# Kernel tuning notes

Hardware: AMD Instinct MI355X
Metric: run time of the kernel (lower is better)

The kernel has to match this reference:

```python
import jax, jax.numpy as jnp
import numpy as np

CAPACITY_FACTOR = 1.0
MIN_CAPACITY = 4


def setup_inputs() -> dict:
    key = jax.random.key(0)
    ks = jax.random.split(key, 4)
    B, S, D, E, F = 4, 2048, 1024, 16, 4096
    hidden_states = jax.random.normal(ks[0], (B, S, D), dtype=jnp.float32)
    wg = jax.random.normal(ks[1], (D, E), dtype=jnp.float32) * 0.02
    w1 = jax.random.normal(ks[2], (E, D, F), dtype=jnp.float32) * (1.0 / np.sqrt(D))
    b1 = jnp.zeros((E, F), dtype=jnp.float32)
    w2 = jax.random.normal(ks[3], (E, F, D), dtype=jnp.float32) * (1.0 / np.sqrt(F))
    b2 = jnp.zeros((E, D), dtype=jnp.float32)
    return {"hidden_states": hidden_states, "wg": wg, "w1": w1, "b1": b1, "w2": w2, "b2": b2}


def reference(hidden_states, wg, w1, b1, w2, b2):
    B, S, D = hidden_states.shape
    x = hidden_states.reshape(-1, D)                      # [T, D] tokens
    T = x.shape[0]
    E = wg.shape[1]
    capacity = max(int(np.ceil(T / E * CAPACITY_FACTOR)), MIN_CAPACITY)  # static

    # ---- TopKGate (k=1, no noise, no RTS) ----
    logits = x @ wg                                       # [T, E]
    gates = jax.nn.softmax(logits, axis=-1)
    idx1 = jnp.argmax(gates, axis=1)                      # [T]
    mask1 = jax.nn.one_hot(idx1, E, dtype=gates.dtype)    # [T, E]
    exp_counts = jnp.sum(mask1, axis=0).astype(jnp.int32) # per-expert token counts

    # load-balancing aux loss
    me = jnp.mean(gates, axis=0)
    ce = jnp.mean(mask1, axis=0)
    l_aux = jnp.sum(me * ce) * E

    # slot assignment within each expert, drop overflow tokens
    locations1 = jnp.cumsum(mask1, axis=0) - 1.0          # [T, E]
    mask1 = mask1 * (locations1 < capacity).astype(gates.dtype)
    locations1_s = jnp.sum(locations1 * mask1, axis=1).astype(jnp.int32)  # [T]
    gates1 = gates * mask1                                # [T, E] gate prob of kept assignment

    loc_oh = jax.nn.one_hot(locations1_s, capacity, dtype=gates.dtype)    # [T, C]
    combine = jnp.einsum('te,tc->tec', gates1, loc_oh)    # [T, E, C]
    dispatch = (combine > 0).astype(x.dtype)              # [T, E, C]

    # ---- dispatch -> grouped expert FFN -> combine ----
    disp = jnp.einsum('tec,td->ecd', dispatch, x)         # [E, C, D]
    h = jax.nn.gelu(jnp.einsum('ecd,edf->ecf', disp, w1) + b1[:, None, :])
    eo = jnp.einsum('ecf,efd->ecd', h, w2) + b2[:, None, :]  # [E, C, D]
    out = jnp.einsum('tec,ecd->td', combine, eo).reshape(B, S, D)
    return out, l_aux, exp_counts
```

## Files before the change

### kernel.cpp

```cpp
#include <hip/hip_runtime.h>

typedef unsigned short u16;
typedef unsigned int   u32;
typedef unsigned long long u64;
typedef __attribute__((ext_vector_type(8))) __bf16 bf16x8;
typedef __attribute__((ext_vector_type(4))) float  f32x4;
typedef __attribute__((ext_vector_type(2))) u32    u32x2;

#define TOK 8192
#define DIM 1024
#define NE  16
#define NF  4096
#define CAP 512

#define BQ  288
#define BG  1184
#define BLSZ 9472

__device__ __forceinline__ u16 f2bf(float f) {
    u32 u = __float_as_uint(f);
    u32 r = (u + 0x7FFFu + ((u >> 16) & 1u)) >> 16;
    return (u16)r;
}

__device__ __forceinline__ float gelu_tanh(float x) {
    float u = 0.7978845608028654f * (x + 0.044715f * x * x * x);
    float t = __expf(-2.f * fabsf(u));
    float th = (1.f - t) / (1.f + t);
    th = (u < 0.f) ? -th : th;
    return 0.5f * x * (1.f + th);
}

__device__ __forceinline__ void gld16(const void* g, void* l) {
    __builtin_amdgcn_global_load_lds(
        (const __attribute__((address_space(1))) void*)g,
        (__attribute__((address_space(3))) void*)l, 16, 0, 0);
}

__device__ __forceinline__ u32 lds_addr(const void* p) {
    return (u32)(uintptr_t)(const __attribute__((address_space(3))) void*)p;
}

#define BFRAG2(BF0, BF1, A0, A1) do { \
    u32x2 l0_, h0_, l1_, h1_; \
    asm volatile("ds_read_b64_tr_b16 %0, %4\n\t" \
                 "ds_read_b64_tr_b16 %1, %4 offset:128\n\t" \
                 "ds_read_b64_tr_b16 %2, %5\n\t" \
                 "ds_read_b64_tr_b16 %3, %5 offset:128\n\t" \
                 "s_waitcnt lgkmcnt(0)" \
                 : "=&v"(l0_), "=&v"(h0_), "=&v"(l1_), "=&v"(h1_) \
                 : "v"(A0), "v"(A1) : "memory"); \
    union { u32 u[4]; bf16x8 v; } c0_, c1_; \
    c0_.u[0] = l0_[0]; c0_.u[1] = l0_[1]; c0_.u[2] = h0_[0]; c0_.u[3] = h0_[1]; \
    c1_.u[0] = l1_[0]; c1_.u[1] = l1_[1]; c1_.u[2] = h1_[0]; c1_.u[3] = h1_[1]; \
    (BF0) = c0_.v; (BF1) = c1_.v; } while (0)

__global__ void moe_wgT(const float* __restrict__ wg, float* __restrict__ wgT,
                        float* __restrict__ me_sums) {
    int i = blockIdx.x * 256 + threadIdx.x;
    if (i < NE) me_sums[i] = 0.f;
    int d = i >> 4, e = i & 15;
    wgT[(size_t)e * DIM + d] = wg[i];
}

__global__ void moe_gate(const float* __restrict__ x, const float* __restrict__ wgT,
                         int* __restrict__ eidx, float* __restrict__ gp,
                         float* __restrict__ me_sums) {
    __shared__ float lme[NE];
    const int tid = threadIdx.x;
    if (tid < NE) lme[tid] = 0.f;
    __syncthreads();
    const int tok = blockIdx.x * 16 + (tid >> 4);
    const int e   = tid & 15;
    const float4* xp = (const float4*)(x + (size_t)tok * DIM);
    const float4* wp = (const float4*)(wgT + (size_t)e * DIM);
    float acc = 0.f;
#pragma unroll 4
    for (int i = 0; i < DIM / 4; ++i) {
        float4 a = xp[i], b = wp[i];
        acc = fmaf(a.x, b.x, acc); acc = fmaf(a.y, b.y, acc);
        acc = fmaf(a.z, b.z, acc); acc = fmaf(a.w, b.w, acc);
    }
    float mx = acc;
    for (int off = 8; off; off >>= 1) mx = fmaxf(mx, __shfl_xor(mx, off, 16));
    float ex = __expf(acc - mx);
    float sum = ex;
    for (int off = 8; off; off >>= 1) sum += __shfl_xor(sum, off, 16);
    float p = ex / sum;
    atomicAdd(&lme[e], p);
    float bv = acc; int bi = e;
    for (int off = 8; off; off >>= 1) {
        float ov = __shfl_xor(bv, off, 16);
        int   oi = __shfl_xor(bi, off, 16);
        if (ov > bv || (ov == bv && oi < bi)) { bv = ov; bi = oi; }
    }
    float pw = __shfl(p, bi, 16);
    if (e == 0) { eidx[tok] = bi; gp[tok] = pw; }
    __syncthreads();
    if (tid < 16) atomicAdd(&me_sums[tid], lme[tid]);
}

__global__ void moe_scan(const int* __restrict__ eidx, const float* __restrict__ me_sums,
                         int* __restrict__ slot, int* __restrict__ tos,
                         float* __restrict__ tail ) {
    __shared__ int wcnt[16][16];
    __shared__ int base[16];
    const int tid = threadIdx.x, wid = tid >> 6, lane = tid & 63;
    if (tid < 16) base[tid] = 0;
    for (int i = tid; i < NE * CAP; i += 1024) tos[i] = -1;
    __syncthreads();
    const u64 below = ((u64)1 << lane) - 1;
    for (int chunk = 0; chunk < TOK / 1024; ++chunk) {
        int t = chunk * 1024 + tid;
        int e = eidx[t];
        int rank = 0;
#pragma unroll
        for (int ex = 0; ex < 16; ++ex) {
            u64 m = __ballot(e == ex);
            if (e == ex)    rank = __popcll(m & below);
            if (lane == ex) wcnt[wid][ex] = __popcll(m);
        }
        __syncthreads();
        int pre = base[e];
        for (int w = 0; w < wid; ++w) pre += wcnt[w][e];
        int s = pre + rank;
        slot[t] = s;
        if (s < CAP) tos[e * CAP + s] = t;
        __syncthreads();
        if (tid < 16) {
            int tot = 0;
            for (int w = 0; w < 16; ++w) tot += wcnt[w][tid];
            base[tid] += tot;
        }
        __syncthreads();
    }
    if (tid == 0) {
        float laux = 0.f;
        for (int e2 = 0; e2 < 16; ++e2) {
            float me = me_sums[e2] / (float)TOK;
            float ce = (float)base[e2] / (float)TOK;
            laux += me * ce;
        }
        tail[0] = laux * (float)NE;
    }
    if (tid < 16) tail[1 + tid] = (float)base[tid];
}

__global__ void moe_gather_zero(const float* __restrict__ x, const int* __restrict__ tos,
                                const int* __restrict__ slot, u16* __restrict__ Xg,
                                float* __restrict__ out) {
    const int b = blockIdx.x, tid = threadIdx.x;
    const int t = tos[b];
    float4 v = make_float4(0.f, 0.f, 0.f, 0.f);
    if (t >= 0) v = *(const float4*)(x + (size_t)t * DIM + tid * 4);
    u32 lo = (u32)f2bf(v.x) | ((u32)f2bf(v.y) << 16);
    u32 hi = (u32)f2bf(v.z) | ((u32)f2bf(v.w) << 16);
    *(uint2*)(Xg + (size_t)b * DIM + tid * 4) = make_uint2(lo, hi);
    if (slot[b] >= CAP)
        *(float4*)(out + (size_t)b * DIM + tid * 4) = make_float4(0.f, 0.f, 0.f, 0.f);
}

__global__ __launch_bounds__(512, 4) void moe_gemm1(const u16* __restrict__ Xg,
                                                    const float* __restrict__ w1,
                                                    const float* __restrict__ b1,
                                                    u16* __restrict__ H) {
    __shared__ alignas(16) u16 Als[2][8192];
    __shared__ alignas(16) u16 Bls[2][BLSZ / 2];
    const int tid = threadIdx.x, wave = tid >> 6, lane = tid & 63;
    const int flat = blockIdx.x;
    const int xcd  = flat & 7;
    const int slot = flat >> 3;
    const int e    = xcd * 2 + (slot >> 6);
    const int tile = slot & 63;
    const int bm   = tile & 1;
    const int bn   = tile >> 1;
    const int r4   = lane >> 2;
    const int gch  = (lane & 3) ^ ((lane >> 3) & 3);
    const u16* aSrc = Xg + (size_t)(e * 512 + bm * 256 + wave * 16 + r4) * DIM + gch * 8;
    const int bk = tid >> 4, bn8 = tid & 15;
    const float* bSrc = w1 + ((size_t)e * DIM + bk) * NF + bn * 128 + bn8 * 8;
    const int bwoff = (bn8 >> 1) * BG + (bk >> 3) * BQ + (bk & 7) * 32 + (bn8 & 1) * 16;
    const int wm = wave & 1, wn = wave >> 1;
    const int fr = lane & 15, fq = lane >> 4;
    const int rdoff = fr * 32 + (fq ^ ((fr >> 1) & 3)) * 8;
    const u32 ldsB = lds_addr(&Bls[0][0]);
    const int btr0 = (wn * 2 + 0) * BG + fq * BQ + fr * 2;
    const int btr1 = (wn * 2 + 1) * BG + fq * BQ + fr * 2;

    f32x4 acc[2][4][2] = {};
    float4 q0, q1;

#define STGA1(P, T) do { const int ko = (T) * 32; \
        u16* ad = &Als[P][wave * 512]; \
        gld16(aSrc + ko, ad); gld16(aSrc + 128 * DIM + ko, ad + 4096); } while (0)
#define BWR1(P) do { \
        u32 p0 = (u32)f2bf(q0.x) | ((u32)f2bf(q0.y) << 16); \
        u32 p1 = (u32)f2bf(q0.z) | ((u32)f2bf(q0.w) << 16); \
        u32 p2 = (u32)f2bf(q1.x) | ((u32)f2bf(q1.y) << 16); \
        u32 p3 = (u32)f2bf(q1.z) | ((u32)f2bf(q1.w) << 16); \
        *(uint4*)((char*)&Bls[0][0] + (P) * BLSZ + bwoff) = make_uint4(p0, p1, p2, p3); } while (0)

    const int NT = DIM / 32;
    STGA1(0, 0);
    q0 = *(const float4*)(bSrc); q1 = *(const float4*)(bSrc + 4);
    asm volatile("s_waitcnt vmcnt(0)" ::: "memory");
    BWR1(0);
    asm volatile("s_waitcnt lgkmcnt(0)" ::: "memory");
    __builtin_amdgcn_s_barrier();
    for (int t = 0; t < NT; ++t) {
        const int buf = t & 1;
        if (t + 1 < NT) {
            STGA1(buf ^ 1, t + 1);
            const float* s = bSrc + (size_t)(t + 1) * (32 * NF);
            q0 = *(const float4*)(s); q1 = *(const float4*)(s + 4);
        }
        bf16x8 aF[4], bF[2];
        const u32 bb = ldsB + buf * BLSZ;
        BFRAG2(bF[0], bF[1], bb + btr0, bb + btr1);
        const u16* Ab = &Als[buf][0];
#pragma unroll
        for (int i = 0; i < 4; ++i)
            aF[i] = *(const bf16x8*)(const void*)(Ab + (wm * 128 + i * 16) * 32 + rdoff);
        __builtin_amdgcn_sched_barrier(0);
        __builtin_amdgcn_s_setprio(1);
#pragma unroll
        for (int i = 0; i < 4; ++i)
#pragma unroll
            for (int j = 0; j < 2; ++j)
                acc[0][i][j] = __builtin_amdgcn_mfma_f32_16x16x32_bf16(aF[i], bF[j], acc[0][i][j], 0, 0, 0);
        __builtin_amdgcn_s_setprio(0);
#pragma unroll
        for (int i = 0; i < 4; ++i)
            aF[i] = *(const bf16x8*)(const void*)(Ab + (wm * 128 + 64 + i * 16) * 32 + rdoff);
        __builtin_amdgcn_s_setprio(1);
#pragma unroll
        for (int i = 0; i < 4; ++i)
#pragma unroll
            for (int j = 0; j < 2; ++j)
                acc[1][i][j] = __builtin_amdgcn_mfma_f32_16x16x32_bf16(aF[i], bF[j], acc[1][i][j], 0, 0, 0);
        __builtin_amdgcn_s_setprio(0);
        if (t + 1 < NT) {
            asm volatile("s_waitcnt vmcnt(0)" ::: "memory");
            BWR1(buf ^ 1);
        }
        asm volatile("s_waitcnt lgkmcnt(0)" ::: "memory");
        __builtin_amdgcn_s_barrier();
    }
#undef STGA1
#undef BWR1

    const int mBase = e * 512 + bm * 256 + wm * 128;
    const int nBase = bn * 128 + wn * 32;
#pragma unroll
    for (int j = 0; j < 2; ++j) {
        const int f = nBase + j * 16 + fr;
        const float bias = b1[e * NF + f];
#pragma unroll
        for (int q = 0; q < 2; ++q)
#pragma unroll
            for (int i = 0; i < 4; ++i) {
                const int m0 = mBase + q * 64 + i * 16 + fq * 4;
#pragma unroll
                for (int r = 0; r < 4; ++r) {
                    float v = acc[q][i][j][r] + bias;
                    H[(size_t)(m0 + r) * NF + f] = f2bf(gelu_tanh(v));
                }
            }
    }
}

__global__ __launch_bounds__(512, 4) void moe_gemm2(const u16* __restrict__ H,
                                                    const float* __restrict__ w2,
                                                    const float* __restrict__ b2,
                                                    const int* __restrict__ tos,
                                                    const float* __restrict__ gp,
                                                    float* __restrict__ out) {
    __shared__ alignas(16) u16 Als[2][8192];
    __shared__ alignas(16) u16 Bls[2][BLSZ / 2];
    const int tid = threadIdx.x, wave = tid >> 6, lane = tid & 63;
    const int flat = blockIdx.x;
    const int xcd  = flat & 7;
    const int slot = flat >> 3;
    const int e    = xcd * 2 + (slot >> 4);
    const int tile = slot & 15;
    const int bm   = tile & 1;
    const int bn   = tile >> 1;
    const int r4   = lane >> 2;
    const int gch  = (lane & 3) ^ ((lane >> 3) & 3);
    const u16* aSrc = H + (size_t)(e * 512 + bm * 256 + wave * 16 + r4) * NF + gch * 8;
    const int bk = tid >> 4, bn8 = tid & 15;
    const float* bSrc = w2 + ((size_t)e * NF + bk) * DIM + bn * 128 + bn8 * 8;
    const int bwoff = (bn8 >> 1) * BG + (bk >> 3) * BQ + (bk & 7) * 32 + (bn8 & 1) * 16;
    const int wm = wave & 1, wn = wave >> 1;
    const int fr = lane & 15, fq = lane >> 4;
    const int rdoff = fr * 32 + (fq ^ ((fr >> 1) & 3)) * 8;
    const u32 ldsB = lds_addr(&Bls[0][0]);
    const int btr0 = (wn * 2 + 0) * BG + fq * BQ + fr * 2;
    const int btr1 = (wn * 2 + 1) * BG + fq * BQ + fr * 2;

    f32x4 acc[2][4][2] = {};
    float4 q0, q1;

#define STGA2(P, T) do { const int ko = (T) * 32; \
        u16* ad = &Als[P][wave * 512]; \
        gld16(aSrc + ko, ad); gld16(aSrc + (size_t)128 * NF + ko, ad + 4096); } while (0)
#define BWR2(P) do { \
        u32 p0 = (u32)f2bf(q0.x) | ((u32)f2bf(q0.y) << 16); \
        u32 p1 = (u32)f2bf(q0.z) | ((u32)f2bf(q0.w) << 16); \
        u32 p2 = (u32)f2bf(q1.x) | ((u32)f2bf(q1.y) << 16); \
        u32 p3 = (u32)f2bf(q1.z) | ((u32)f2bf(q1.w) << 16); \
        *(uint4*)((char*)&Bls[0][0] + (P) * BLSZ + bwoff) = make_uint4(p0, p1, p2, p3); } while (0)

    const int NT = NF / 32;
    STGA2(0, 0);
    q0 = *(const float4*)(bSrc); q1 = *(const float4*)(bSrc + 4);
    asm volatile("s_waitcnt vmcnt(0)" ::: "memory");
    BWR2(0);
    asm volatile("s_waitcnt lgkmcnt(0)" ::: "memory");
    __builtin_amdgcn_s_barrier();
    for (int t = 0; t < NT; ++t) {
        const int buf = t & 1;
        if (t + 1 < NT) {
            STGA2(buf ^ 1, t + 1);
            const float* s = bSrc + (size_t)(t + 1) * (32 * DIM);
            q0 = *(const float4*)(s); q1 = *(const float4*)(s + 4);
        }
        bf16x8 aF[4], bF[2];
        const u32 bb = ldsB + buf * BLSZ;
        BFRAG2(bF[0], bF[1], bb + btr0, bb + btr1);
        const u16* Ab = &Als[buf][0];
#pragma unroll
        for (int i = 0; i < 4; ++i)
            aF[i] = *(const bf16x8*)(const void*)(Ab + (wm * 128 + i * 16) * 32 + rdoff);
        __builtin_amdgcn_sched_barrier(0);
        __builtin_amdgcn_s_setprio(1);
#pragma unroll
        for (int i = 0; i < 4; ++i)
#pragma unroll
            for (int j = 0; j < 2; ++j)
                acc[0][i][j] = __builtin_amdgcn_mfma_f32_16x16x32_bf16(aF[i], bF[j], acc[0][i][j], 0, 0, 0);
        __builtin_amdgcn_s_setprio(0);
#pragma unroll
        for (int i = 0; i < 4; ++i)
            aF[i] = *(const bf16x8*)(const void*)(Ab + (wm * 128 + 64 + i * 16) * 32 + rdoff);
        __builtin_amdgcn_s_setprio(1);
#pragma unroll
        for (int i = 0; i < 4; ++i)
#pragma unroll
            for (int j = 0; j < 2; ++j)
                acc[1][i][j] = __builtin_amdgcn_mfma_f32_16x16x32_bf16(aF[i], bF[j], acc[1][i][j], 0, 0, 0);
        __builtin_amdgcn_s_setprio(0);
        if (t + 1 < NT) {
            asm volatile("s_waitcnt vmcnt(0)" ::: "memory");
            BWR2(buf ^ 1);
        }
        asm volatile("s_waitcnt lgkmcnt(0)" ::: "memory");
        __builtin_amdgcn_s_barrier();
    }
#undef STGA2
#undef BWR2

    const int mBase = e * 512 + bm * 256 + wm * 128;
    const int nBase = bn * 128 + wn * 32;
#pragma unroll
    for (int q = 0; q < 2; ++q)
#pragma unroll
        for (int i = 0; i < 4; ++i) {
#pragma unroll
            for (int r = 0; r < 4; ++r) {
                const int m = mBase + q * 64 + i * 16 + fq * 4 + r;
                const int t = tos[m];
                if (t < 0) continue;
                const float g = gp[t];
#pragma unroll
                for (int j = 0; j < 2; ++j) {
                    const int d = nBase + j * 16 + fr;
                    out[(size_t)t * DIM + d] = g * (acc[q][i][j][r] + b2[e * DIM + d]);
                }
            }
        }
}

extern "C" void kernel_launch(void* const* d_in, const int* in_sizes, int n_in,
                              void* d_out, int out_size, void* d_ws, size_t ws_size,
                              hipStream_t stream) {
    const float* x  = (const float*)d_in[0];
    const float* wg = (const float*)d_in[1];
    const float* w1 = (const float*)d_in[2];
    const float* b1 = (const float*)d_in[3];
    const float* w2 = (const float*)d_in[4];
    const float* b2 = (const float*)d_in[5];
    float* out = (float*)d_out;

    char* ws = (char*)d_ws;
    const size_t XG_OFF = 0;
    const size_t H_OFF  = XG_OFF + (size_t)TOK * DIM * 2;
    const size_t SM_OFF = H_OFF + (size_t)TOK * NF * 2;
    u16* Xg = (u16*)(ws + XG_OFF);
    u16* H  = (u16*)(ws + H_OFF);
    int*   eidx = (int*)(ws + SM_OFF);
    float* gp   = (float*)(ws + SM_OFF + 32768);
    int*   slot = (int*)(ws + SM_OFF + 65536);
    int*   tos  = (int*)(ws + SM_OFF + 98304);
    float* me   = (float*)(ws + SM_OFF + 131072);
    float* wgT  = (float*)(ws + SM_OFF + 131072 + 128);

    float* tail = out + (size_t)TOK * DIM;

    moe_wgT<<<64, 256, 0, stream>>>(wg, wgT, me);
    moe_gate<<<TOK / 16, 256, 0, stream>>>(x, wgT, eidx, gp, me);
    moe_scan<<<1, 1024, 0, stream>>>(eidx, me, slot, tos, tail);
    moe_gather_zero<<<NE * CAP, 256, 0, stream>>>(x, tos, slot, Xg, out);
    moe_gemm1<<<1024, 512, 0, stream>>>(Xg, w1, b1, H);
    moe_gemm2<<<256, 512, 0, stream>>>(H, w2, b2, tos, gp, out);
}
```

Baseline: 808.5 us.

## Deepen GEMM pipelines to four stages with transposed scalar weight loads

Both expert GEMM kernels move from double-buffered LDS staging to a four-slot ring, keeping three K-tiles of loads in flight, with partial vmcnt waits in place of full drains. The fp32 weight tile is now read as eight strided scalar loads per thread, so each thread writes its bf16 values to LDS already K-contiguous. This lets the B fragment be read with ordinary vector LDS reads instead of ds_read_b64_tr_b16 transposing reads. The larger LDS footprint lowers the occupancy hint from 4 to 2 blocks per CU, and the strided scalar global loads may coalesce worse than the earlier float4 loads.

```diff
diff --git a/kernel.cpp b/kernel.cpp
--- a/kernel.cpp
+++ b/kernel.cpp
@@ -5,17 +5,12 @@
 typedef unsigned long long u64;
 typedef __attribute__((ext_vector_type(8))) __bf16 bf16x8;
 typedef __attribute__((ext_vector_type(4))) float  f32x4;
-typedef __attribute__((ext_vector_type(2))) u32    u32x2;
 
 #define TOK 8192
 #define DIM 1024
 #define NE  16
 #define NF  4096
 #define CAP 512
-
-#define BQ  288
-#define BG  1184
-#define BLSZ 9472
 
 __device__ __forceinline__ u16 f2bf(float f) {
     u32 u = __float_as_uint(f);
@@ -36,24 +31,6 @@
         (const __attribute__((address_space(1))) void*)g,
         (__attribute__((address_space(3))) void*)l, 16, 0, 0);
 }
-
-__device__ __forceinline__ u32 lds_addr(const void* p) {
-    return (u32)(uintptr_t)(const __attribute__((address_space(3))) void*)p;
-}
-
-#define BFRAG2(BF0, BF1, A0, A1) do { \
-    u32x2 l0_, h0_, l1_, h1_; \
-    asm volatile("ds_read_b64_tr_b16 %0, %4\n\t" \
-                 "ds_read_b64_tr_b16 %1, %4 offset:128\n\t" \
-                 "ds_read_b64_tr_b16 %2, %5\n\t" \
-                 "ds_read_b64_tr_b16 %3, %5 offset:128\n\t" \
-                 "s_waitcnt lgkmcnt(0)" \
-                 : "=&v"(l0_), "=&v"(h0_), "=&v"(l1_), "=&v"(h1_) \
-                 : "v"(A0), "v"(A1) : "memory"); \
-    union { u32 u[4]; bf16x8 v; } c0_, c1_; \
-    c0_.u[0] = l0_[0]; c0_.u[1] = l0_[1]; c0_.u[2] = h0_[0]; c0_.u[3] = h0_[1]; \
-    c1_.u[0] = l1_[0]; c1_.u[1] = l1_[1]; c1_.u[2] = h1_[0]; c1_.u[3] = h1_[1]; \
-    (BF0) = c0_.v; (BF1) = c1_.v; } while (0)
 
 __global__ void moe_wgT(const float* __restrict__ wg, float* __restrict__ wgT,
                         float* __restrict__ me_sums) {
@@ -160,12 +137,12 @@
         *(float4*)(out + (size_t)b * DIM + tid * 4) = make_float4(0.f, 0.f, 0.f, 0.f);
 }
 
-__global__ __launch_bounds__(512, 4) void moe_gemm1(const u16* __restrict__ Xg,
+__global__ __launch_bounds__(512, 2) void moe_gemm1(const u16* __restrict__ Xg,
                                                     const float* __restrict__ w1,
                                                     const float* __restrict__ b1,
                                                     u16* __restrict__ H) {
-    __shared__ alignas(16) u16 Als[2][8192];
-    __shared__ alignas(16) u16 Bls[2][BLSZ / 2];
+    __shared__ alignas(16) u16 Als[4][8192];
+    __shared__ alignas(16) u16 Bls[4][4096];
     const int tid = threadIdx.x, wave = tid >> 6, lane = tid & 63;
     const int flat = blockIdx.x;
     const int xcd  = flat & 7;
@@ -177,77 +154,82 @@
     const int r4   = lane >> 2;
     const int gch  = (lane & 3) ^ ((lane >> 3) & 3);
     const u16* aSrc = Xg + (size_t)(e * 512 + bm * 256 + wave * 16 + r4) * DIM + gch * 8;
-    const int bk = tid >> 4, bn8 = tid & 15;
-    const float* bSrc = w1 + ((size_t)e * DIM + bk) * NF + bn * 128 + bn8 * 8;
-    const int bwoff = (bn8 >> 1) * BG + (bk >> 3) * BQ + (bk & 7) * 32 + (bn8 & 1) * 16;
+    const float* bSrc = w1 + (size_t)e * DIM * NF + (size_t)gch * 8 * NF
+                      + (bn * 128 + wave * 16 + r4);
     const int wm = wave & 1, wn = wave >> 1;
     const int fr = lane & 15, fq = lane >> 4;
     const int rdoff = fr * 32 + (fq ^ ((fr >> 1) & 3)) * 8;
-    const u32 ldsB = lds_addr(&Bls[0][0]);
-    const int btr0 = (wn * 2 + 0) * BG + fq * BQ + fr * 2;
-    const int btr1 = (wn * 2 + 1) * BG + fq * BQ + fr * 2;
 
     f32x4 acc[2][4][2] = {};
-    float4 q0, q1;
-
-#define STGA1(P, T) do { const int ko = (T) * 32; \
-        u16* ad = &Als[P][wave * 512]; \
-        gld16(aSrc + ko, ad); gld16(aSrc + 128 * DIM + ko, ad + 4096); } while (0)
-#define BWR1(P) do { \
-        u32 p0 = (u32)f2bf(q0.x) | ((u32)f2bf(q0.y) << 16); \
-        u32 p1 = (u32)f2bf(q0.z) | ((u32)f2bf(q0.w) << 16); \
-        u32 p2 = (u32)f2bf(q1.x) | ((u32)f2bf(q1.y) << 16); \
-        u32 p3 = (u32)f2bf(q1.z) | ((u32)f2bf(q1.w) << 16); \
-        *(uint4*)((char*)&Bls[0][0] + (P) * BLSZ + bwoff) = make_uint4(p0, p1, p2, p3); } while (0)
-
-    const int NT = DIM / 32;
-    STGA1(0, 0);
-    q0 = *(const float4*)(bSrc); q1 = *(const float4*)(bSrc + 4);
-    asm volatile("s_waitcnt vmcnt(0)" ::: "memory");
+    float q[4][8];
+    const int NT1 = DIM / 32;
+
+#define ISSUE1(T, S) do { const int ko_ = (T) * 32; \
+        u16* ad_ = &Als[(T) & 3][wave * 512]; \
+        gld16(aSrc + ko_, ad_); gld16(aSrc + 128 * DIM + ko_, ad_ + 4096); \
+        const float* bs_ = bSrc + (size_t)ko_ * NF; \
+        _Pragma("unroll") for (int i_ = 0; i_ < 8; ++i_) q[S][i_] = bs_[(size_t)i_ * NF]; \
+    } while (0)
+#define BWR1(S) do { \
+        u32 p0_ = (u32)f2bf(q[S][0]) | ((u32)f2bf(q[S][1]) << 16); \
+        u32 p1_ = (u32)f2bf(q[S][2]) | ((u32)f2bf(q[S][3]) << 16); \
+        u32 p2_ = (u32)f2bf(q[S][4]) | ((u32)f2bf(q[S][5]) << 16); \
+        u32 p3_ = (u32)f2bf(q[S][6]) | ((u32)f2bf(q[S][7]) << 16); \
+        *(uint4*)(&Bls[S][tid * 8]) = make_uint4(p0_, p1_, p2_, p3_); \
+    } while (0)
+#define COMP1(CUR) do { \
+        const u16* Ab_ = &Als[CUR][0]; \
+        const u16* Bb_ = &Bls[CUR][0]; \
+        bf16x8 aF_[4], bF_[2]; \
+        _Pragma("unroll") for (int j_ = 0; j_ < 2; ++j_) \
+            bF_[j_] = *(const bf16x8*)(const void*)(Bb_ + (wn * 32 + j_ * 16) * 32 + rdoff); \
+        _Pragma("unroll") for (int i_ = 0; i_ < 4; ++i_) \
+            aF_[i_] = *(const bf16x8*)(const void*)(Ab_ + (wm * 128 + i_ * 16) * 32 + rdoff); \
+        __builtin_amdgcn_s_setprio(1); \
+        _Pragma("unroll") for (int i_ = 0; i_ < 4; ++i_) \
+        _Pragma("unroll") for (int j_ = 0; j_ < 2; ++j_) \
+            acc[0][i_][j_] = __builtin_amdgcn_mfma_f32_16x16x32_bf16(aF_[i_], bF_[j_], acc[0][i_][j_], 0, 0, 0); \
+        __builtin_amdgcn_s_setprio(0); \
+        _Pragma("unroll") for (int i_ = 0; i_ < 4; ++i_) \
+            aF_[i_] = *(const bf16x8*)(const void*)(Ab_ + (wm * 128 + 64 + i_ * 16) * 32 + rdoff); \
+        __builtin_amdgcn_s_setprio(1); \
+        _Pragma("unroll") for (int i_ = 0; i_ < 4; ++i_) \
+        _Pragma("unroll") for (int j_ = 0; j_ < 2; ++j_) \
+            acc[1][i_][j_] = __builtin_amdgcn_mfma_f32_16x16x32_bf16(aF_[i_], bF_[j_], acc[1][i_][j_], 0, 0, 0); \
+        __builtin_amdgcn_s_setprio(0); \
+    } while (0)
+#define STEP1(T, CUR, NXT, ISS) do { \
+        if ((T) + 3 < NT1) ISSUE1((T) + 3, ISS); \
+        if ((T) + 1 < NT1) { \
+            if ((T) + 3 < NT1)      asm volatile("s_waitcnt vmcnt(20)" ::: "memory"); \
+            else if ((T) + 2 < NT1) asm volatile("s_waitcnt vmcnt(10)" ::: "memory"); \
+            else                    asm volatile("s_waitcnt vmcnt(0)"  ::: "memory"); \
+            BWR1(NXT); \
+        } \
+        asm volatile("s_waitcnt lgkmcnt(0)" ::: "memory"); \
+        __builtin_amdgcn_sched_barrier(0); \
+        __builtin_amdgcn_s_barrier(); \
+        __builtin_amdgcn_sched_barrier(0); \
+        COMP1(CUR); \
+        __builtin_amdgcn_sched_barrier(0); \
+        __builtin_amdgcn_s_barrier(); \
+    } while (0)
+
+    ISSUE1(0, 0); ISSUE1(1, 1); ISSUE1(2, 2);
+    asm volatile("s_waitcnt vmcnt(20)" ::: "memory");
     BWR1(0);
     asm volatile("s_waitcnt lgkmcnt(0)" ::: "memory");
     __builtin_amdgcn_s_barrier();
-    for (int t = 0; t < NT; ++t) {
-        const int buf = t & 1;
-        if (t + 1 < NT) {
-            STGA1(buf ^ 1, t + 1);
-            const float* s = bSrc + (size_t)(t + 1) * (32 * NF);
-            q0 = *(const float4*)(s); q1 = *(const float4*)(s + 4);
-        }
-        bf16x8 aF[4], bF[2];
-        const u32 bb = ldsB + buf * BLSZ;
-        BFRAG2(bF[0], bF[1], bb + btr0, bb + btr1);
-        const u16* Ab = &Als[buf][0];
-#pragma unroll
-        for (int i = 0; i < 4; ++i)
-            aF[i] = *(const bf16x8*)(const void*)(Ab + (wm * 128 + i * 16) * 32 + rdoff);
-        __builtin_amdgcn_sched_barrier(0);
-        __builtin_amdgcn_s_setprio(1);
-#pragma unroll
-        for (int i = 0; i < 4; ++i)
-#pragma unroll
-            for (int j = 0; j < 2; ++j)
-                acc[0][i][j] = __builtin_amdgcn_mfma_f32_16x16x32_bf16(aF[i], bF[j], acc[0][i][j], 0, 0, 0);
-        __builtin_amdgcn_s_setprio(0);
-#pragma unroll
-        for (int i = 0; i < 4; ++i)
-            aF[i] = *(const bf16x8*)(const void*)(Ab + (wm * 128 + 64 + i * 16) * 32 + rdoff);
-        __builtin_amdgcn_s_setprio(1);
-#pragma unroll
-        for (int i = 0; i < 4; ++i)
-#pragma unroll
-            for (int j = 0; j < 2; ++j)
-                acc[1][i][j] = __builtin_amdgcn_mfma_f32_16x16x32_bf16(aF[i], bF[j], acc[1][i][j], 0, 0, 0);
-        __builtin_amdgcn_s_setprio(0);
-        if (t + 1 < NT) {
-            asm volatile("s_waitcnt vmcnt(0)" ::: "memory");
-            BWR1(buf ^ 1);
-        }
-        asm volatile("s_waitcnt lgkmcnt(0)" ::: "memory");
-        __builtin_amdgcn_s_barrier();
-    }
-#undef STGA1
+    for (int T = 0; T < NT1; T += 4) {
+        STEP1(T + 0, 0, 1, 3);
+        STEP1(T + 1, 1, 2, 0);
+        STEP1(T + 2, 2, 3, 1);
+        STEP1(T + 3, 3, 0, 2);
+    }
+#undef ISSUE1
 #undef BWR1
+#undef COMP1
+#undef STEP1
 
     const int mBase = e * 512 + bm * 256 + wm * 128;
     const int nBase = bn * 128 + wn * 32;
@@ -256,27 +238,27 @@
         const int f = nBase + j * 16 + fr;
         const float bias = b1[e * NF + f];
 #pragma unroll
-        for (int q = 0; q < 2; ++q)
+        for (int qq = 0; qq < 2; ++qq)
 #pragma unroll
             for (int i = 0; i < 4; ++i) {
-                const int m0 = mBase + q * 64 + i * 16 + fq * 4;
+                const int m0 = mBase + qq * 64 + i * 16 + fq * 4;
 #pragma unroll
                 for (int r = 0; r < 4; ++r) {
-                    float v = acc[q][i][j][r] + bias;
+                    float v = acc[qq][i][j][r] + bias;
                     H[(size_t)(m0 + r) * NF + f] = f2bf(gelu_tanh(v));
                 }
             }
     }
 }
 
-__global__ __launch_bounds__(512, 4) void moe_gemm2(const u16* __restrict__ H,
+__global__ __launch_bounds__(512, 2) void moe_gemm2(const u16* __restrict__ H,
                                                     const float* __restrict__ w2,
                                                     const float* __restrict__ b2,
                                                     const int* __restrict__ tos,
                                                     const float* __restrict__ gp,
                                                     float* __restrict__ out) {
-    __shared__ alignas(16) u16 Als[2][8192];
-    __shared__ alignas(16) u16 Bls[2][BLSZ / 2];
+    __shared__ alignas(16) u16 Als[4][8192];
+    __shared__ alignas(16) u16 Bls[4][4096];
     const int tid = threadIdx.x, wave = tid >> 6, lane = tid & 63;
     const int flat = blockIdx.x;
     const int xcd  = flat & 7;
@@ -288,94 +270,99 @@
     const int r4   = lane >> 2;
     const int gch  = (lane & 3) ^ ((lane >> 3) & 3);
     const u16* aSrc = H + (size_t)(e * 512 + bm * 256 + wave * 16 + r4) * NF + gch * 8;
-    const int bk = tid >> 4, bn8 = tid & 15;
-    const float* bSrc = w2 + ((size_t)e * NF + bk) * DIM + bn * 128 + bn8 * 8;
-    const int bwoff = (bn8 >> 1) * BG + (bk >> 3) * BQ + (bk & 7) * 32 + (bn8 & 1) * 16;
+    const float* bSrc = w2 + (size_t)e * NF * DIM + (size_t)gch * 8 * DIM
+                      + (bn * 128 + wave * 16 + r4);
     const int wm = wave & 1, wn = wave >> 1;
     const int fr = lane & 15, fq = lane >> 4;
     const int rdoff = fr * 32 + (fq ^ ((fr >> 1) & 3)) * 8;
-    const u32 ldsB = lds_addr(&Bls[0][0]);
-    const int btr0 = (wn * 2 + 0) * BG + fq * BQ + fr * 2;
-    const int btr1 = (wn * 2 + 1) * BG + fq * BQ + fr * 2;
 
     f32x4 acc[2][4][2] = {};
-    float4 q0, q1;
-
-#define STGA2(P, T) do { const int ko = (T) * 32; \
-        u16* ad = &Als[P][wave * 512]; \
-        gld16(aSrc + ko, ad); gld16(aSrc + (size_t)128 * NF + ko, ad + 4096); } while (0)
-#define BWR2(P) do { \
-        u32 p0 = (u32)f2bf(q0.x) | ((u32)f2bf(q0.y) << 16); \
-        u32 p1 = (u32)f2bf(q0.z) | ((u32)f2bf(q0.w) << 16); \
-        u32 p2 = (u32)f2bf(q1.x) | ((u32)f2bf(q1.y) << 16); \
-        u32 p3 = (u32)f2bf(q1.z) | ((u32)f2bf(q1.w) << 16); \
-        *(uint4*)((char*)&Bls[0][0] + (P) * BLSZ + bwoff) = make_uint4(p0, p1, p2, p3); } while (0)
-
-    const int NT = NF / 32;
-    STGA2(0, 0);
-    q0 = *(const float4*)(bSrc); q1 = *(const float4*)(bSrc + 4);
-    asm volatile("s_waitcnt vmcnt(0)" ::: "memory");
+    float q[4][8];
+    const int NT2 = NF / 32;
+
+#define ISSUE2(T, S) do { const int ko_ = (T) * 32; \
+        u16* ad_ = &Als[(T) & 3][wave * 512]; \
+        gld16(aSrc + ko_, ad_); gld16(aSrc + (size_t)128 * NF + ko_, ad_ + 4096); \
+        const float* bs_ = bSrc + (size_t)ko_ * DIM; \
+        _Pragma("unroll") for (int i_ = 0; i_ < 8; ++i_) q[S][i_] = bs_[(size_t)i_ * DIM]; \
+    } while (0)
+#define BWR2(S) do { \
+        u32 p0_ = (u32)f2bf(q[S][0]) | ((u32)f2bf(q[S][1]) << 16); \
+        u32 p1_ = (u32)f2bf(q[S][2]) | ((u32)f2bf(q[S][3]) << 16); \
+        u32 p2_ = (u32)f2bf(q[S][4]) | ((u32)f2bf(q[S][5]) << 16); \
+        u32 p3_ = (u32)f2bf(q[S][6]) | ((u32)f2bf(q[S][7]) << 16); \
+        *(uint4*)(&Bls[S][tid * 8]) = make_uint4(p0_, p1_, p2_, p3_); \
+    } while (0)
+#define COMP2(CUR) do { \
+        const u16* Ab_ = &Als[CUR][0]; \
+        const u16* Bb_ = &Bls[CUR][0]; \
+        bf16x8 aF_[4], bF_[2]; \
+        _Pragma("unroll") for (int j_ = 0; j_ < 2; ++j_) \
+            bF_[j_] = *(const bf16x8*)(const void*)(Bb_ + (wn * 32 + j_ * 16) * 32 + rdoff); \
+        _Pragma("unroll") for (int i_ = 0; i_ < 4; ++i_) \
+            aF_[i_] = *(const bf16x8*)(const void*)(Ab_ + (wm * 128 + i_ * 16) * 32 + rdoff); \
+        __builtin_amdgcn_s_setprio(1); \
+        _Pragma("unroll") for (int i_ = 0; i_ < 4; ++i_) \
+        _Pragma("unroll") for (int j_ = 0; j_ < 2; ++j_) \
+            acc[0][i_][j_] = __builtin_amdgcn_mfma_f32_16x16x32_bf16(aF_[i_], bF_[j_], acc[0][i_][j_], 0, 0, 0); \
+        __builtin_amdgcn_s_setprio(0); \
+        _Pragma("unroll") for (int i_ = 0; i_ < 4; ++i_) \
+            aF_[i_] = *(const bf16x8*)(const void*)(Ab_ + (wm * 128 + 64 + i_ * 16) * 32 + rdoff); \
+        __builtin_amdgcn_s_setprio(1); \
+        _Pragma("unroll") for (int i_ = 0; i_ < 4; ++i_) \
+        _Pragma("unroll") for (int j_ = 0; j_ < 2; ++j_) \
+            acc[1][i_][j_] = __builtin_amdgcn_mfma_f32_16x16x32_bf16(aF_[i_], bF_[j_], acc[1][i_][j_], 0, 0, 0); \
+        __builtin_amdgcn_s_setprio(0); \
+    } while (0)
+#define STEP2(T, CUR, NXT, ISS) do { \
+        if ((T) + 3 < NT2) ISSUE2((T) + 3, ISS); \
+        if ((T) + 1 < NT2) { \
+            if ((T) + 3 < NT2)      asm volatile("s_waitcnt vmcnt(20)" ::: "memory"); \
+            else if ((T) + 2 < NT2) asm volatile("s_waitcnt vmcnt(10)" ::: "memory"); \
+            else                    asm volatile("s_waitcnt vmcnt(0)"  ::: "memory"); \
+            BWR2(NXT); \
+        } \
+        asm volatile("s_waitcnt lgkmcnt(0)" ::: "memory"); \
+        __builtin_amdgcn_sched_barrier(0); \
+        __builtin_amdgcn_s_barrier(); \
+        __builtin_amdgcn_sched_barrier(0); \
+        COMP2(CUR); \
+        __builtin_amdgcn_sched_barrier(0); \
+        __builtin_amdgcn_s_barrier(); \
+    } while (0)
+
+    ISSUE2(0, 0); ISSUE2(1, 1); ISSUE2(2, 2);
+    asm volatile("s_waitcnt vmcnt(20)" ::: "memory");
     BWR2(0);
     asm volatile("s_waitcnt lgkmcnt(0)" ::: "memory");
     __builtin_amdgcn_s_barrier();
-    for (int t = 0; t < NT; ++t) {
-        const int buf = t & 1;
-        if (t + 1 < NT) {
-            STGA2(buf ^ 1, t + 1);
-            const float* s = bSrc + (size_t)(t + 1) * (32 * DIM);
-            q0 = *(const float4*)(s); q1 = *(const float4*)(s + 4);
-        }
-        bf16x8 aF[4], bF[2];
-        const u32 bb = ldsB + buf * BLSZ;
-        BFRAG2(bF[0], bF[1], bb + btr0, bb + btr1);
-        const u16* Ab = &Als[buf][0];
-#pragma unroll
-        for (int i = 0; i < 4; ++i)
-            aF[i] = *(const bf16x8*)(const void*)(Ab + (wm * 128 + i * 16) * 32 + rdoff);
-        __builtin_amdgcn_sched_barrier(0);
-        __builtin_amdgcn_s_setprio(1);
-#pragma unroll
-        for (int i = 0; i < 4; ++i)
-#pragma unroll
-            for (int j = 0; j < 2; ++j)
-                acc[0][i][j] = __builtin_amdgcn_mfma_f32_16x16x32_bf16(aF[i], bF[j], acc[0][i][j], 0, 0, 0);
-        __builtin_amdgcn_s_setprio(0);
-#pragma unroll
-        for (int i = 0; i < 4; ++i)
-            aF[i] = *(const bf16x8*)(const void*)(Ab + (wm * 128 + 64 + i * 16) * 32 + rdoff);
-        __builtin_amdgcn_s_setprio(1);
-#pragma unroll
-        for (int i = 0; i < 4; ++i)
-#pragma unroll
-            for (int j = 0; j < 2; ++j)
-                acc[1][i][j] = __builtin_amdgcn_mfma_f32_16x16x32_bf16(aF[i], bF[j], acc[1][i][j], 0, 0, 0);
-        __builtin_amdgcn_s_setprio(0);
-        if (t + 1 < NT) {
-            asm volatile("s_waitcnt vmcnt(0)" ::: "memory");
-            BWR2(buf ^ 1);
-        }
-        asm volatile("s_waitcnt lgkmcnt(0)" ::: "memory");
-        __builtin_amdgcn_s_barrier();
-    }
-#undef STGA2
+    for (int T = 0; T < NT2; T += 4) {
+        STEP2(T + 0, 0, 1, 3);
+        STEP2(T + 1, 1, 2, 0);
+        STEP2(T + 2, 2, 3, 1);
+        STEP2(T + 3, 3, 0, 2);
+    }
+#undef ISSUE2
 #undef BWR2
+#undef COMP2
+#undef STEP2
 
     const int mBase = e * 512 + bm * 256 + wm * 128;
     const int nBase = bn * 128 + wn * 32;
 #pragma unroll
-    for (int q = 0; q < 2; ++q)
+    for (int qq = 0; qq < 2; ++qq)
 #pragma unroll
         for (int i = 0; i < 4; ++i) {
 #pragma unroll
             for (int r = 0; r < 4; ++r) {
-                const int m = mBase + q * 64 + i * 16 + fq * 4 + r;
+                const int m = mBase + qq * 64 + i * 16 + fq * 4 + r;
                 const int t = tos[m];
                 if (t < 0) continue;
                 const float g = gp[t];
 #pragma unroll
                 for (int j = 0; j < 2; ++j) {
                     const int d = nBase + j * 16 + fr;
-                    out[(size_t)t * DIM + d] = g * (acc[q][i][j][r] + b2[e * DIM + d]);
+                    out[(size_t)t * DIM + d] = g * (acc[qq][i][j][r] + b2[e * DIM + d]);
                 }
             }
         }
```

Result: slower. 923.9 us (+14.3%).
